# Kernel optimization log

Hardware: AMD Instinct MI355X
Metric: run time of the kernel (lower is better)

The kernel has to match this reference:

```python
import jax, jax.numpy as jnp
import numpy as np

B, L, G, HID, H, D = 2, 4096, 256, 768, 12, 64
R = 127            # local_radius
BLK = R + 1        # block_len = 128
N = L // BLK       # 32 blocks (L divisible by BLK)
W = 2 * R + 1      # 255 local window
V = 32             # relative vocab size


def setup_inputs() -> dict:
    ks = jax.random.split(jax.random.key(0), 40)
    inp = {}
    inp["long_input"] = jax.random.normal(ks[0], (B, L, HID), jnp.float32)
    inp["global_input"] = jax.random.normal(ks[1], (B, G, HID), jnp.float32)
    inp["l2l_att_mask"] = jax.random.randint(ks[2], (B, L, W), 0, 2, jnp.int32)
    inp["g2g_att_mask"] = jax.random.randint(ks[3], (B, G, G), 0, 2, jnp.int32)
    inp["l2g_att_mask"] = jax.random.randint(ks[4], (B, L, G), 0, 2, jnp.int32)
    inp["g2l_att_mask"] = jax.random.randint(ks[5], (B, G, L), 0, 2, jnp.int32)
    inp["l2l_relative_att_ids"] = jax.random.randint(ks[6], (B, L, W), 0, V, jnp.int32)
    inp["g2g_relative_att_ids"] = jax.random.randint(ks[7], (B, G, G), 0, V, jnp.int32)
    inp["l2g_relative_att_ids"] = jax.random.randint(ks[8], (B, L, G), 0, V, jnp.int32)
    inp["g2l_relative_att_ids"] = jax.random.randint(ks[9], (B, G, L), 0, V, jnp.int32)
    i = 10
    for nm in ["q_long", "k_long", "v_long", "q_glob", "k_glob", "v_glob"]:
        inp["w" + nm] = 0.02 * jax.random.normal(ks[i], (HID, H * D), jnp.float32); i += 1
        inp["b" + nm] = jnp.zeros((H * D,), jnp.float32)
    inp["rel_emb_long"] = 0.5 * jax.random.normal(ks[i], (V, H, D), jnp.float32); i += 1
    inp["rel_bias_long"] = jnp.zeros((V, H), jnp.float32)
    inp["rel_emb_glob"] = 0.5 * jax.random.normal(ks[i], (V, H, D), jnp.float32); i += 1
    inp["rel_bias_glob"] = jnp.zeros((V, H), jnp.float32)
    inp["wo_long"] = 0.02 * jax.random.normal(ks[i], (H * D, HID), jnp.float32); i += 1
    inp["bo_long"] = jnp.zeros((HID,), jnp.float32)
    inp["wo_glob"] = 0.02 * jax.random.normal(ks[i], (H * D, HID), jnp.float32); i += 1
    inp["bo_glob"] = jnp.zeros((HID,), jnp.float32)
    return inp


def _expand_local(x):
    """[B, L, W] local-window ids -> blocked [B, N, BLK, 3*BLK] (skew + pad),
    zeroing entries outside the local window or outside the sequence."""
    xb = x.reshape(B, N, BLK, W)
    p = jnp.arange(BLK)[:, None]        # query pos within block
    c = jnp.arange(3 * BLK)[None, :]    # key pos within 3-block window
    r = c - p - 1                       # index into the 2R+1 window
    valid = (r >= 0) & (r < W)
    rc = jnp.clip(r, 0, W - 1)
    out = jnp.take_along_axis(xb, jnp.broadcast_to(rc, (B, N, BLK, 3 * BLK)), axis=-1)
    j = (jnp.arange(N)[:, None, None] - 1) * BLK + c  # absolute key position
    valid_full = valid[None] & (j >= 0) & (j < L)     # [N, BLK, 3*BLK]
    return out * valid_full[None].astype(x.dtype)


def reference(long_input, global_input,
              l2l_att_mask, g2g_att_mask, l2g_att_mask, g2l_att_mask,
              l2l_relative_att_ids, g2g_relative_att_ids,
              l2g_relative_att_ids, g2l_relative_att_ids,
              wq_long, bq_long, wk_long, bk_long, wv_long, bv_long,
              wq_glob, bq_glob, wk_glob, bk_glob, wv_glob, bv_glob,
              rel_emb_long, rel_bias_long, rel_emb_glob, rel_bias_glob,
              wo_long, bo_long, wo_glob, bo_glob):
    scale = 1.0 / jnp.sqrt(jnp.float32(D))

    def proj(x, w, b):
        return (x @ w + b).reshape(x.shape[0], x.shape[1], H, D)

    lq, lk, lv = proj(long_input, wq_long, bq_long), proj(long_input, wk_long, bk_long), proj(long_input, wv_long, bv_long)
    gq, gk, gv = proj(global_input, wq_glob, bq_glob), proj(global_input, wk_glob, bk_glob), proj(global_input, wv_glob, bv_glob)

    # ---- long tokens: blocked local attention fused with side (global) keys ----
    qb = lq.reshape(B, N, BLK, H, D)

    def concat3(x):
        xb = x.reshape(B, N, BLK, H, D)
        pad = jnp.zeros_like(xb[:, :1])
        xp = jnp.concatenate([pad, xb, pad], axis=1)  # [B, N+2, BLK, H, D]
        return jnp.concatenate([xp[:, :-2], xp[:, 1:-1], xp[:, 2:]], axis=2)  # [B,N,3BLK,H,D]

    keys = jnp.concatenate([concat3(lk), jnp.broadcast_to(gk[:, None], (B, N, G, H, D))], axis=2)
    vals = jnp.concatenate([concat3(lv), jnp.broadcast_to(gv[:, None], (B, N, G, H, D))], axis=2)

    mask = jnp.concatenate([_expand_local(l2l_att_mask), l2g_att_mask.reshape(B, N, BLK, G)], axis=-1)
    ids = jnp.concatenate([_expand_local(l2l_relative_att_ids), l2g_relative_att_ids.reshape(B, N, BLK, G)], axis=-1)

    scores = jnp.einsum('bnqhd,bnkhd->bnqkh', qb, keys)
    rel_all = jnp.einsum('bnqhd,rhd->bnqrh', qb, rel_emb_long) + rel_bias_long
    rel = jnp.take_along_axis(rel_all, jnp.broadcast_to(ids[..., None], ids.shape + (H,)), axis=3)
    scores = (scores + rel) * scale
    scores = scores - 10000.0 * (1.0 - mask[..., None].astype(scores.dtype))
    probs = jax.nn.softmax(scores, axis=3)
    long_ctx = jnp.einsum('bnqkh,bnkhd->bnqhd', probs, vals).reshape(B, L, H * D)
    long_out = long_ctx @ wo_long + bo_long

    # ---- global tokens: full attention over [global; long] keys ----
    kf = jnp.concatenate([gk, lk], axis=1)
    vf = jnp.concatenate([gv, lv], axis=1)
    gmask = jnp.concatenate([g2g_att_mask, g2l_att_mask], axis=-1)
    gids = jnp.concatenate([g2g_relative_att_ids, g2l_relative_att_ids], axis=-1)
    gs = jnp.einsum('bqhd,bkhd->bqkh', gq, kf)
    grel_all = jnp.einsum('bqhd,rhd->bqrh', gq, rel_emb_glob) + rel_bias_glob
    grel = jnp.take_along_axis(grel_all, jnp.broadcast_to(gids[..., None], gids.shape + (H,)), axis=2)
    gs = (gs + grel) * scale
    gs = gs - 10000.0 * (1.0 - gmask[..., None].astype(gs.dtype))
    gp = jax.nn.softmax(gs, axis=2)
    glob_ctx = jnp.einsum('bqkh,bkhd->bqhd', gp, vf).reshape(B, G, H * D)
    glob_out = glob_ctx @ wo_glob + bo_glob

    return long_out, glob_out
```

## Files before the change

kernel.cpp:

```cpp
#include <hip/hip_runtime.h>
#include <hip/hip_bf16.h>

typedef unsigned short u16;
typedef unsigned char u8;
typedef unsigned int u32;
typedef __attribute__((ext_vector_type(8))) short bf16x8;
typedef __attribute__((ext_vector_type(4))) float f32x4;

#define BB 2
#define LL 4096
#define GG 256
#define HH 12
#define DD 64
#define NB 32
#define WW 255
#define VV 32
#define NCHUNK 17
#define LKEY 640
#define GKEY 4352
#define WMAT 589824

#define PKL_BLK 20480
#define PKG_BLK 8704
#define WPR_BLK 1152
#define XPL_BLK 3072
#define XPG_BLK 192

__device__ __forceinline__ float bf2f(u16 u) {
  return __uint_as_float(((unsigned)u) << 16);
}
__device__ __forceinline__ u16 f2bf(float f) {
  unsigned u = __float_as_uint(f);
  u += 0x7FFFu + ((u >> 16) & 1u);
  return (u16)(u >> 16);
}
__device__ __forceinline__ float4 ld4bf(const u16* p) {
  ushort4 q = *reinterpret_cast<const ushort4*>(p);
  return make_float4(bf2f(q.x), bf2f(q.y), bf2f(q.z), bf2f(q.w));
}
__device__ __forceinline__ float ldx1(const void* p, size_t idx, bool f32m) {
  if (f32m) return reinterpret_cast<const float*>(p)[idx];
  return bf2f(reinterpret_cast<const u16*>(p)[idx]);
}
__device__ __forceinline__ void gload16(const u16* src, u16* ldsdst) {
  __builtin_amdgcn_global_load_lds(
      (const __attribute__((address_space(1))) unsigned int*)src,
      (__attribute__((address_space(3))) unsigned int*)ldsdst, 16, 0, 0);
}

__global__ void detect_dtype(const void* __restrict__ x, int* __restrict__ flag) {
  __shared__ int cnt;
  if (threadIdx.x == 0) cnt = 0;
  __syncthreads();
  const u16* p = reinterpret_cast<const u16*>(x);
  int c = 0;
  for (int i = threadIdx.x; i < 4096; i += 256) {
    int e = (p[i] >> 7) & 0xFF;
    if (e >= 134) c++;
  }
  atomicAdd(&cnt, c);
  __syncthreads();
  if (threadIdx.x == 0) *flag = (cnt >= 64) ? 1 : 0;
}

__global__ __launch_bounds__(256)
void prep(const int* __restrict__ m_l2l, const int* __restrict__ m_l2g,
          const int* __restrict__ i_l2l, const int* __restrict__ i_l2g,
          const int* __restrict__ m_g2g, const int* __restrict__ m_g2l,
          const int* __restrict__ i_g2g, const int* __restrict__ i_g2l,
          u8* __restrict__ pkl, u8* __restrict__ pkg,
          const void* __restrict__ W0, const void* __restrict__ W1,
          const void* __restrict__ W2, const void* __restrict__ W3,
          const void* __restrict__ W4, const void* __restrict__ W5,
          const void* __restrict__ W6, const void* __restrict__ W7,
          u16* __restrict__ wtq, u16* __restrict__ wto,
          const void* __restrict__ xlin, const void* __restrict__ xgin,
          u16* __restrict__ xl, u16* __restrict__ xg,
          const int* __restrict__ flagp) {
  __shared__ u16 T[64][72];
  const bool f32m = (*flagp != 0);
  const int tid = threadIdx.x;
  const int bid = blockIdx.x;

  if (bid < PKL_BLK) {
    const unsigned idx = (unsigned)bid * 256u + tid;
    const int pos = idx & 63;
    const int lnp = pos >> 2, ktp = pos & 3;
    const int qrow = (idx >> 6) & 127;
    const unsigned rest = idx >> 13;
    const int tile = rest % 10;
    const unsigned bn = rest / 10;
    const int n = bn & 31, b = bn >> 5;
    const int c = (tile << 6) + (ktp << 4) + lnp;
    const unsigned bt = (unsigned)b * LL + (n << 7) + qrow;
    int mask = 0, id = 0;
    if (c < 384) {
      const int rr = c - qrow - 1;
      const int jabs = ((n - 1) << 7) + c;
      if (rr >= 0 && rr < WW && jabs >= 0 && jabs < LL) {
        const size_t base = (size_t)bt * WW + rr;
        mask = m_l2l[base]; id = i_l2l[base];
      }
    } else {
      const size_t base = (size_t)bt * GG + (c - 384);
      mask = m_l2g[base]; id = i_l2g[base];
    }
    pkl[idx] = (u8)((id & 31) | ((mask ^ 1) << 7));
  } else if (bid < PKL_BLK + PKG_BLK) {
    const unsigned idx = (unsigned)(bid - PKL_BLK) * 256u + tid;
    const int pos = idx & 63;
    const int lnp = pos >> 2, ktp = pos & 3;
    const int qrow = (idx >> 6) & 127;
    const unsigned rest = idx >> 13;
    const int tl = rest % 68;
    const unsigned b2q = rest / 68;
    const int b = b2q >> 1, qtp = b2q & 1;
    const int c = (tl << 6) + (ktp << 4) + lnp;
    const int q = (qtp << 7) + qrow;
    int mask, id;
    if (c < 256) {
      const size_t base = ((size_t)b * GG + q) * GG + c;
      mask = m_g2g[base]; id = i_g2g[base];
    } else {
      const size_t base = ((size_t)b * GG + q) * (size_t)LL + (c - 256);
      mask = m_g2l[base]; id = i_g2l[base];
    }
    pkg[idx] = (u8)((id & 31) | ((mask ^ 1) << 7));
  } else if (bid < PKL_BLK + PKG_BLK + WPR_BLK) {
    const int blk = bid - (PKL_BLK + PKG_BLK);
    const int mat = blk / 144;
    const int rem = blk % 144;
    const int n0 = (rem % 12) << 6, k0 = (rem / 12) << 6;
    const void* Wm = (mat == 0) ? W0 : (mat == 1) ? W1 : (mat == 2) ? W2
                     : (mat == 3) ? W3 : (mat == 4) ? W4 : (mat == 5) ? W5
                     : (mat == 6) ? W6 : W7;
    u16* wbase = (mat < 6) ? (wtq + (size_t)mat * WMAT)
                           : (wto + (size_t)(mat - 6) * WMAT);
    {
      const int r = tid >> 2, c0 = (tid & 3) << 4;
      if (f32m) {
        const float* wp = reinterpret_cast<const float*>(Wm) + (size_t)(k0 + r) * 768 + n0 + c0;
        #pragma unroll
        for (int j = 0; j < 16; j += 4) {
          float4 v = *reinterpret_cast<const float4*>(wp + j);
          T[r][c0 + j + 0] = f2bf(v.x); T[r][c0 + j + 1] = f2bf(v.y);
          T[r][c0 + j + 2] = f2bf(v.z); T[r][c0 + j + 3] = f2bf(v.w);
        }
      } else {
        const u16* wp = reinterpret_cast<const u16*>(Wm) + (size_t)(k0 + r) * 768 + n0 + c0;
        *reinterpret_cast<int4*>(&T[r][c0]) = reinterpret_cast<const int4*>(wp)[0];
        *reinterpret_cast<int4*>(&T[r][c0 + 8]) = reinterpret_cast<const int4*>(wp)[1];
      }
    }
    __syncthreads();
    {
      const int n = tid >> 2, kc0 = (tid & 3) << 4;
      u16 buf[16];
      #pragma unroll
      for (int j = 0; j < 16; j++) buf[j] = T[kc0 + j][n];
      u16* op = wbase + (size_t)(n0 + n) * 768 + k0 + kc0;
      *reinterpret_cast<int4*>(op) = *reinterpret_cast<int4*>(buf);
      *reinterpret_cast<int4*>(op + 8) = *reinterpret_cast<int4*>(buf + 8);
    }
  } else {
    const int blk = bid - (PKL_BLK + PKG_BLK + WPR_BLK);
    const void* src;
    u16* dst;
    size_t i;
    if (blk < XPL_BLK) {
      src = xlin; dst = xl;
      i = ((size_t)blk * 256 + tid) << 3;
    } else {
      src = xgin; dst = xg;
      i = ((size_t)(blk - XPL_BLK) * 256 + tid) << 3;
    }
    if (f32m) {
      const float* p = reinterpret_cast<const float*>(src) + i;
      float4 a = *reinterpret_cast<const float4*>(p);
      float4 b = *reinterpret_cast<const float4*>(p + 4);
      u16 o[8] = {f2bf(a.x), f2bf(a.y), f2bf(a.z), f2bf(a.w),
                  f2bf(b.x), f2bf(b.y), f2bf(b.z), f2bf(b.w)};
      *reinterpret_cast<int4*>(dst + i) = *reinterpret_cast<int4*>(o);
    } else {
      *reinterpret_cast<int4*>(dst + i) =
          *reinterpret_cast<const int4*>(reinterpret_cast<const u16*>(src) + i);
    }
  }
}

#define GEMM_CORE(A_, Wt_, row0_, ncol0_)                                        \
  __shared__ u16 lds[16384];                                                     \
  const int tid = threadIdx.x;                                                   \
  const int w = tid >> 6, l = tid & 63;                                          \
  const int lm = l & 15, quad = l >> 4;                                          \
  const int wr = w >> 1, wc = w & 1;                                             \
  const int rb = (w << 5) + (l >> 3);                                            \
  const int c8 = (l & 7) ^ (l >> 3);                                             \
  const u16* asrc = A_ + (size_t)(row0_ + rb) * 768 + (c8 << 3);                 \
  const u16* bsrc = Wt_ + (size_t)(ncol0_ + rb) * 768 + (c8 << 3);               \
  u16* adst = lds + (w << 11) + (l << 3);                                        \
  u16* bdst = adst + 8192;                                                       \
  f32x4 acc[4][4];                                                               \
  _Pragma("unroll")                                                              \
  for (int mt = 0; mt < 4; mt++)                                                 \
    _Pragma("unroll")                                                            \
    for (int nt = 0; nt < 4; nt++) acc[mt][nt] = (f32x4){0.f, 0.f, 0.f, 0.f};    \
  const char* abase = reinterpret_cast<const char*>(lds);                        \
  const char* bbase = abase + 16384;                                             \
  const int xorv = (lm & 7) << 4;                                                \
  for (int k0 = 0; k0 < 768; k0 += 64) {                                         \
    __syncthreads();                                                             \
    _Pragma("unroll")                                                            \
    for (int i = 0; i < 4; i++) gload16(asrc + k0 + i * 6144, adst + (i << 9));  \
    _Pragma("unroll")                                                            \
    for (int i = 0; i < 4; i++) gload16(bsrc + k0 + i * 6144, bdst + (i << 9));  \
    __syncthreads();                                                             \
    _Pragma("unroll")                                                            \
    for (int kk = 0; kk < 2; kk++) {                                             \
      bf16x8 af[4], bfr[4];                                                      \
      _Pragma("unroll")                                                          \
      for (int mt = 0; mt < 4; mt++)                                             \
        af[mt] = *reinterpret_cast<const bf16x8*>(                               \
            abase + ((wr << 6) + (mt << 4) + lm) * 128 +                         \
            (((kk << 6) + (quad << 4)) ^ xorv));                                 \
      _Pragma("unroll")                                                          \
      for (int nt = 0; nt < 4; nt++)                                             \
        bfr[nt] = *reinterpret_cast<const bf16x8*>(                              \
            bbase + ((wc << 6) + (nt << 4) + lm) * 128 +                         \
            (((kk << 6) + (quad << 4)) ^ xorv));                                 \
      _Pragma("unroll")                                                          \
      for (int mt = 0; mt < 4; mt++)                                             \
        _Pragma("unroll")                                                        \
        for (int nt = 0; nt < 4; nt++)                                           \
          acc[mt][nt] = __builtin_amdgcn_mfma_f32_16x16x32_bf16(                 \
              af[mt], bfr[nt], acc[mt][nt], 0, 0, 0);                            \
    }                                                                            \
  }

__global__ __launch_bounds__(256)
void gemm_qkv(const u16* __restrict__ Al, const u16* __restrict__ Ag,
              const u16* __restrict__ Wtq,
              const void* __restrict__ bql, const void* __restrict__ bkl,
              const void* __restrict__ bvl,
              const void* __restrict__ bqg, const void* __restrict__ bkg,
              const void* __restrict__ bvg,
              u16* __restrict__ lq, u16* __restrict__ lk, u16* __restrict__ lv,
              u16* __restrict__ gq, u16* __restrict__ gk, u16* __restrict__ gv,
              const int* __restrict__ flagp) {
  const bool f32m = (*flagp != 0);
  const int fid = blockIdx.x;
  int lx, ly;
  const u16 *A, *Wt;
  const void *B0, *B1, *B2;
  u16 *C0, *C1, *C2;
  if (fid < 1152) {
    const int x = fid & 7, r = fid >> 3;
    ly = (x << 3) | (r & 7);
    lx = r >> 3;
    A = Al; Wt = Wtq;
    B0 = bql; B1 = bkl; B2 = bvl;
    C0 = lq; C1 = lk; C2 = lv;
  } else {
    const int g = fid - 1152;
    lx = g % 18; ly = g / 18;
    A = Ag; Wt = Wtq + (size_t)3 * WMAT;
    B0 = bqg; B1 = bkg; B2 = bvg;
    C0 = gq; C1 = gk; C2 = gv;
  }
  const int row0 = ly << 7;
  const int ncol0 = lx << 7;
  GEMM_CORE(A, Wt, row0, ncol0)

  const int which = lx / 6;
  const void* bias = (which == 0) ? B0 : ((which == 1) ? B1 : B2);
  u16* Cv = (which == 0) ? C0 : ((which == 1) ? C1 : C2);
  const float sc = (which == 0) ? 0.125f : 1.0f;
  const int colw = (lx % 6) << 7;
  #pragma unroll
  for (int nt = 0; nt < 4; nt++) {
    const int gcol = colw + (wc << 6) + (nt << 4) + lm;
    const float bv = ldx1(bias, gcol, f32m);
    #pragma unroll
    for (int mt = 0; mt < 4; mt++)
      #pragma unroll
      for (int r = 0; r < 4; r++) {
        const int grow = row0 + (wr << 6) + (mt << 4) + (quad << 2) + r;
        Cv[(size_t)grow * 768 + gcol] = f2bf((acc[mt][nt][r] + bv) * sc);
      }
  }
}

__global__ __launch_bounds__(256)
void gemm_out(const u16* __restrict__ Alc, const u16* __restrict__ Agc,
              const u16* __restrict__ Wto,
              const void* __restrict__ bol, const void* __restrict__ bog,
              void* __restrict__ Cv, const int* __restrict__ flagp) {
  const bool f32m = (*flagp != 0);
  const int fid = blockIdx.x;
  int lx, ly;
  const u16 *A, *Wt;
  const void* bias;
  size_t c_off;
  if (fid < 384) {
    const int x = fid & 7, r = fid >> 3;
    ly = (x << 3) | (r & 7);
    lx = r >> 3;
    A = Alc; Wt = Wto; bias = bol; c_off = 0;
  } else {
    const int g = fid - 384;
    lx = g % 6; ly = g / 6;
    A = Agc; Wt = Wto + WMAT; bias = bog; c_off = (size_t)BB * LL * 768;
  }
  const int row0 = ly << 7;
  const int ncol0 = lx << 7;
  GEMM_CORE(A, Wt, row0, ncol0)

  #pragma unroll
  for (int nt = 0; nt < 4; nt++) {
    const int gcol = ncol0 + (wc << 6) + (nt << 4) + lm;
    const float bv = ldx1(bias, gcol, f32m);
    #pragma unroll
    for (int mt = 0; mt < 4; mt++)
      #pragma unroll
      for (int r = 0; r < 4; r++) {
        const int grow = row0 + (wr << 6) + (mt << 4) + (quad << 2) + r;
        const float v = acc[mt][nt][r] + bv;
        if (f32m)
          reinterpret_cast<float*>(Cv)[c_off + (size_t)grow * 768 + gcol] = v;
        else
          reinterpret_cast<u16*>(Cv)[c_off + (size_t)grow * 768 + gcol] = f2bf(v);
      }
  }
}

__global__ __launch_bounds__(256)
void relk(const u16* __restrict__ Ql, const u16* __restrict__ Qg,
          const void* __restrict__ embl, const void* __restrict__ biasl,
          const void* __restrict__ embg, const void* __restrict__ biasg,
          u16* __restrict__ outl, u16* __restrict__ outg,
          const int* __restrict__ flagp) {
  const bool f32m = (*flagp != 0);
  const int bid = blockIdx.x;
  const u16* Q;
  const void *emb, *bias;
  u16* outp;
  int h, b, t0, T;
  if (bid < 1536) {
    b = bid / 768;
    const int rem = bid % 768;
    h = rem / 64;
    t0 = (rem % 64) << 6;
    Q = Ql; emb = embl; bias = biasl; outp = outl; T = LL;
  } else {
    const int g = bid - 1536;
    b = g / 48;
    const int rem = g % 48;
    h = rem / 4;
    t0 = (rem % 4) << 6;
    Q = Qg; emb = embg; bias = biasg; outp = outg; T = GG;
  }
  const int tid = threadIdx.x;
  __shared__ float Qst[64][68];
  __shared__ float Es[64][36];
  #pragma unroll
  for (int i = 0; i < 4; i++) {
    const int idx = tid + (i << 8);
    const int tt = idx >> 4, d = (idx & 15) << 2;
    float4 v = ld4bf(Q + (((size_t)b * T + t0 + tt) * HH + h) * DD + d);
    Qst[d + 0][tt] = v.x; Qst[d + 1][tt] = v.y;
    Qst[d + 2][tt] = v.z; Qst[d + 3][tt] = v.w;
  }
  #pragma unroll
  for (int i = 0; i < 8; i++) {
    const int idx = tid + (i << 8);
    const int r = idx >> 6, d = idx & 63;
    Es[d][r] = ldx1(emb, ((size_t)r * HH + h) * DD + d, f32m);
  }
  __syncthreads();
  const int tq = (tid & 31) << 1;
  const int r0 = (tid >> 5) << 2;
  float acc[2][4] = {};
  #pragma unroll 8
  for (int d = 0; d < 64; d++) {
    float2 qq = *reinterpret_cast<const float2*>(&Qst[d][tq]);
    float4 e = *reinterpret_cast<const float4*>(&Es[d][r0]);
    acc[0][0] += qq.x * e.x; acc[0][1] += qq.x * e.y;
    acc[0][2] += qq.x * e.z; acc[0][3] += qq.x * e.w;
    acc[1][0] += qq.y * e.x; acc[1][1] += qq.y * e.y;
    acc[1][2] += qq.y * e.z; acc[1][3] += qq.y * e.w;
  }
  float bv[4];
  #pragma unroll
  for (int j = 0; j < 4; j++) bv[j] = ldx1(bias, (size_t)(r0 + j) * HH + h, f32m) * 0.125f;
  #pragma unroll
  for (int i = 0; i < 2; i++) {
    ushort4 o;
    o.x = f2bf(acc[i][0] + bv[0]); o.y = f2bf(acc[i][1] + bv[1]);
    o.z = f2bf(acc[i][2] + bv[2]); o.w = f2bf(acc[i][3] + bv[3]);
    *reinterpret_cast<ushort4*>(&outp[(((size_t)b * T + t0 + tq + i) * HH + h) * VV + r0]) = o;
  }
}

__global__ __launch_bounds__(512)
void lattn(const u16* __restrict__ lq, const u16* __restrict__ lk, const u16* __restrict__ lv,
           const u16* __restrict__ gk, const u16* __restrict__ gv,
           const u32* __restrict__ pkl, const u16* __restrict__ rel,
           u16* __restrict__ lctx) {
  const int fid = blockIdx.x + 12 * (blockIdx.y + (blockIdx.z << 5));
  const int hg = fid >> 3;
  const int h = hg % 12;
  const int fl = (fid & 7) + ((hg / 12) << 3);
  const int n = fl & 31, b = fl >> 5;
  const int tid = threadIdx.x;
  __shared__ u16 Kt[64][72];
  __shared__ u16 Vt[64][74];
  __shared__ u16 Pt[128][76];
  __shared__ u16 Rl[128][36];

  const int lane = tid & 63, wv = tid >> 6;
  const int ln = lane & 15, quad = lane >> 4;
  const int tbase = n << 7;

  {
    const int qr = (wv << 4) + (lane >> 2);
    const int seg = (lane & 3) << 3;
    *reinterpret_cast<int4*>(&Rl[qr][seg]) = *reinterpret_cast<const int4*>(
        rel + (((size_t)b * LL + tbase + qr) * HH + h) * VV + seg);
  }

  bf16x8 aq[2];
  {
    const int t = tbase + (wv << 4) + ln;
    const u16* qp = lq + (((size_t)b * LL + t) * HH + h) * DD + (quad << 3);
    aq[0] = *reinterpret_cast<const bf16x8*>(qp);
    aq[1] = *reinterpret_cast<const bf16x8*>(qp + 32);
  }

  const u32* pk32 = pkl + (size_t)(b * 32 + n) * 20480;
  const int skey = tid >> 3, sdg = (tid & 7) << 3;
  const int scol = ((skey & 15) << 2) | (skey >> 4);

  f32x4 Oacc[4];
  #pragma unroll
  for (int dt = 0; dt < 4; dt++) Oacc[dt] = (f32x4){0.f, 0.f, 0.f, 0.f};
  float lpart[4] = {};

  for (int tile = 0; tile < 10; tile++) {
    const int c0 = tile << 6;
    const bool isg = (tile >= 6);

    float badd[16];
    #pragma unroll
    for (int r = 0; r < 4; r++) {
      const int qrow = (wv << 4) + (quad << 2) + r;
      const u32 pw = pk32[(((tile << 7) + qrow) << 4) + ln];
      #pragma unroll
      for (int kt = 0; kt < 4; kt++) {
        const u32 pb = (pw >> (kt << 3)) & 0xFFu;
        const float rv = bf2f(Rl[qrow][pb & 31]);
        badd[(kt << 2) + r] = (pb & 0x80u) ? (rv - 10000.f) : rv;
      }
    }

    __syncthreads();
    {
      int4 kraw = {0, 0, 0, 0}, vraw = {0, 0, 0, 0};
      if (isg) {
        const size_t base = (((size_t)b * GG + (c0 - 384) + skey) * HH + h) * DD + sdg;
        kraw = *reinterpret_cast<const int4*>(gk + base);
        vraw = *reinterpret_cast<const int4*>(gv + base);
      } else {
        const int jabs = ((n - 1) << 7) + c0 + skey;
        if (jabs >= 0 && jabs < LL) {
          const size_t base = (((size_t)b * LL + jabs) * HH + h) * DD + sdg;
          kraw = *reinterpret_cast<const int4*>(lk + base);
          vraw = *reinterpret_cast<const int4*>(lv + base);
        }
      }
      *reinterpret_cast<int4*>(&Kt[skey][sdg]) = kraw;
      u16 vb[8];
      *reinterpret_cast<int4*>(vb) = vraw;
      #pragma unroll
      for (int j = 0; j < 8; j++) Vt[sdg + j][scol] = vb[j];
    }
    __syncthreads();

    f32x4 Sacc[4];
    #pragma unroll
    for (int kt = 0; kt < 4; kt++) Sacc[kt] = (f32x4){0.f, 0.f, 0.f, 0.f};
    __builtin_amdgcn_s_setprio(1);
    #pragma unroll
    for (int kk = 0; kk < 2; kk++) {
      bf16x8 bk[4];
      #pragma unroll
      for (int kt = 0; kt < 4; kt++)
        bk[kt] = *reinterpret_cast<const bf16x8*>(&Kt[(kt << 4) + ln][(kk << 5) + (quad << 3)]);
      #pragma unroll
      for (int kt = 0; kt < 4; kt++)
        Sacc[kt] = __builtin_amdgcn_mfma_f32_16x16x32_bf16(aq[kk], bk[kt], Sacc[kt], 0, 0, 0);
    }
    __builtin_amdgcn_s_setprio(0);

    #pragma unroll
    for (int r = 0; r < 4; r++) {
      const int ql = (wv << 4) + (quad << 2) + r;
      const float p0 = __expf(Sacc[0][r] + badd[0 + r]);
      const float p1 = __expf(Sacc[1][r] + badd[4 + r]);
      const float p2 = __expf(Sacc[2][r] + badd[8 + r]);
      const float p3 = __expf(Sacc[3][r] + badd[12 + r]);
      u32 w0, w1;
      asm("v_cvt_pk_bf16_f32 %0, %1, %2" : "=v"(w0) : "v"(p0), "v"(p1));
      asm("v_cvt_pk_bf16_f32 %0, %1, %2" : "=v"(w1) : "v"(p2), "v"(p3));
      uint2 wp; wp.x = w0; wp.y = w1;
      *reinterpret_cast<uint2*>(&Pt[ql][ln << 2]) = wp;
      lpart[r] += (p0 + p1) + (p2 + p3);
    }

    __builtin_amdgcn_s_setprio(1);
    #pragma unroll
    for (int kk = 0; kk < 2; kk++) {
      bf16x8 ap = *reinterpret_cast<const bf16x8*>(&Pt[(wv << 4) + ln][(kk << 5) + (quad << 3)]);
      #pragma unroll
      for (int dt = 0; dt < 4; dt++) {
        bf16x8 bv = *reinterpret_cast<const bf16x8*>(&Vt[(dt << 4) + ln][(kk << 5) + (quad << 3)]);
        Oacc[dt] = __builtin_amdgcn_mfma_f32_16x16x32_bf16(ap, bv, Oacc[dt], 0, 0, 0);
      }
    }
    __builtin_amdgcn_s_setprio(0);
  }

  #pragma unroll
  for (int r = 0; r < 4; r++) {
    float v = lpart[r];
    v += __shfl_xor(v, 1); v += __shfl_xor(v, 2);
    v += __shfl_xor(v, 4); v += __shfl_xor(v, 8);
    const float inv = 1.0f / v;
    const int t = tbase + (wv << 4) + (quad << 2) + r;
    const size_t base = (((size_t)b * LL + t) * HH + h) * DD;
    #pragma unroll
    for (int dt = 0; dt < 4; dt++)
      lctx[base + (dt << 4) + ln] = f2bf(Oacc[dt][r] * inv);
  }
}

__global__ __launch_bounds__(512)
void gattn(const u16* __restrict__ gq, const u16* __restrict__ gk, const u16* __restrict__ gv,
           const u16* __restrict__ lk, const u16* __restrict__ lv,
           const u32* __restrict__ pkg, const u16* __restrict__ relg,
           float* __restrict__ po, float* __restrict__ pl) {
  const int fid = blockIdx.x;
  const int x = fid & 7;
  const int slot = fid >> 3;
  const int qtp = slot & 1;
  const int g = ((slot >> 1) << 3) | x;
  const int h = g % 12;
  const int cb = g / 12;
  const int chunk = cb % 17;
  const int b = cb / 17;
  const int tid = threadIdx.x;
  __shared__ u16 Kt[64][72];
  __shared__ u16 Vt[64][74];
  __shared__ u16 Pt[128][76];
  __shared__ u16 Rg[128][36];

  const int lane = tid & 63, wv = tid >> 6;
  const int ln = lane & 15, quad = lane >> 4;
  const int qbase = qtp << 7;
  const int kbase = chunk << 8;
  const bool isgg = (chunk == 0);

  {
    const int qr = (wv << 4) + (lane >> 2);
    const int seg = (lane & 3) << 3;
    *reinterpret_cast<int4*>(&Rg[qr][seg]) = *reinterpret_cast<const int4*>(
        relg + (((size_t)b * GG + qbase + qr) * HH + h) * VV + seg);
  }

  bf16x8 aq[2];
  {
    const int qa = qbase + (wv << 4) + ln;
    const u16* qp = gq + (((size_t)b * GG + qa) * HH + h) * DD + (quad << 3);
    aq[0] = *reinterpret_cast<const bf16x8*>(qp);
    aq[1] = *reinterpret_cast<const bf16x8*>(qp + 32);
  }

  const u32* pk32 = pkg + (size_t)((b << 1) + qtp) * 139264;
  const int skey = tid >> 3, sdg = (tid & 7) << 3;
  const int scol = ((skey & 15) << 2) | (skey >> 4);

  f32x4 Oacc[4];
  #pragma unroll
  for (int dt = 0; dt < 4; dt++) Oacc[dt] = (f32x4){0.f, 0.f, 0.f, 0.f};
  float lpart[4] = {};

  for (int tile = 0; tile < 4; tile++) {
    const int tl = (chunk << 2) + tile;

    float badd[16];
    #pragma unroll
    for (int r = 0; r < 4; r++) {
      const int qrow = (wv << 4) + (quad << 2) + r;
      const u32 pw = pk32[(((tl << 7) + qrow) << 4) + ln];
      #pragma unroll
      for (int kt = 0; kt < 4; kt++) {
        const u32 pb = (pw >> (kt << 3)) & 0xFFu;
        const float rv = bf2f(Rg[qrow][pb & 31]);
        badd[(kt << 2) + r] = (pb & 0x80u) ? (rv - 10000.f) : rv;
      }
    }

    __syncthreads();
    {
      const int kc = kbase + (tile << 6) + skey;
      int4 kraw, vraw;
      if (isgg) {
        const size_t base = (((size_t)b * GG + kc) * HH + h) * DD + sdg;
        kraw = *reinterpret_cast<const int4*>(gk + base);
        vraw = *reinterpret_cast<const int4*>(gv + base);
      } else {
        const size_t base = (((size_t)b * LL + (kc - 256)) * HH + h) * DD + sdg;
        kraw = *reinterpret_cast<const int4*>(lk + base);
        vraw = *reinterpret_cast<const int4*>(lv + base);
      }
      *reinterpret_cast<int4*>(&Kt[skey][sdg]) = kraw;
      u16 vb[8];
      *reinterpret_cast<int4*>(vb) = vraw;
      #pragma unroll
      for (int j = 0; j < 8; j++) Vt[sdg + j][scol] = vb[j];
    }
    __syncthreads();

    f32x4 Sacc[4];
    #pragma unroll
    for (int kt = 0; kt < 4; kt++) Sacc[kt] = (f32x4){0.f, 0.f, 0.f, 0.f};
    __builtin_amdgcn_s_setprio(1);
    #pragma unroll
    for (int kk = 0; kk < 2; kk++) {
      bf16x8 bk[4];
      #pragma unroll
      for (int kt = 0; kt < 4; kt++)
        bk[kt] = *reinterpret_cast<const bf16x8*>(&Kt[(kt << 4) + ln][(kk << 5) + (quad << 3)]);
      #pragma unroll
      for (int kt = 0; kt < 4; kt++)
        Sacc[kt] = __builtin_amdgcn_mfma_f32_16x16x32_bf16(aq[kk], bk[kt], Sacc[kt], 0, 0, 0);
    }
    __builtin_amdgcn_s_setprio(0);

    #pragma unroll
    for (int r = 0; r < 4; r++) {
      const int ql = (wv << 4) + (quad << 2) + r;
      const float p0 = __expf(Sacc[0][r] + badd[0 + r]);
      const float p1 = __expf(Sacc[1][r] + badd[4 + r]);
      const float p2 = __expf(Sacc[2][r] + badd[8 + r]);
      const float p3 = __expf(Sacc[3][r] + badd[12 + r]);
      u32 w0, w1;
      asm("v_cvt_pk_bf16_f32 %0, %1, %2" : "=v"(w0) : "v"(p0), "v"(p1));
      asm("v_cvt_pk_bf16_f32 %0, %1, %2" : "=v"(w1) : "v"(p2), "v"(p3));
      uint2 wp; wp.x = w0; wp.y = w1;
      *reinterpret_cast<uint2*>(&Pt[ql][ln << 2]) = wp;
      lpart[r] += (p0 + p1) + (p2 + p3);
    }

    __builtin_amdgcn_s_setprio(1);
    #pragma unroll
    for (int kk = 0; kk < 2; kk++) {
      bf16x8 ap = *reinterpret_cast<const bf16x8*>(&Pt[(wv << 4) + ln][(kk << 5) + (quad << 3)]);
      #pragma unroll
      for (int dt = 0; dt < 4; dt++) {
        bf16x8 bv = *reinterpret_cast<const bf16x8*>(&Vt[(dt << 4) + ln][(kk << 5) + (quad << 3)]);
        Oacc[dt] = __builtin_amdgcn_mfma_f32_16x16x32_bf16(ap, bv, Oacc[dt], 0, 0, 0);
      }
    }
    __builtin_amdgcn_s_setprio(0);
  }

  #pragma unroll
  for (int r = 0; r < 4; r++) {
    float v = lpart[r];
    v += __shfl_xor(v, 1); v += __shfl_xor(v, 2);
    v += __shfl_xor(v, 4); v += __shfl_xor(v, 8);
    const int qa = qbase + (wv << 4) + (quad << 2) + r;
    if (ln == 0)
      pl[(((size_t)chunk * BB + b) * HH + h) * GG + qa] = v;
    const size_t base = ((((size_t)chunk * BB + b) * HH + h) * GG + qa) * DD;
    #pragma unroll
    for (int dt = 0; dt < 4; dt++)
      po[base + (dt << 4) + ln] = Oacc[dt][r];
  }
}

__global__ __launch_bounds__(256)
void gcombine(const float* __restrict__ po, const float* __restrict__ pl,
              u16* __restrict__ gctx) {
  const int flat = blockIdx.x * 256 + threadIdx.x;
  const int d = flat & 63;
  const int rest = flat >> 6;
  const int h = rest % HH;
  const int bq = rest / HH;
  const int b = bq >> 8, qg = bq & 255;
  float so = 0.f, sl = 0.f;
  #pragma unroll
  for (int c = 0; c < NCHUNK; c++) {
    so += po[((((size_t)c * BB + b) * HH + h) * GG + qg) * DD + d];
    sl += pl[(((size_t)c * BB + b) * HH + h) * GG + qg];
  }
  gctx[flat] = f2bf(so / sl);
}

extern "C" void kernel_launch(void* const* d_in, const int* in_sizes, int n_in,
                              void* d_out, int out_size, void* d_ws, size_t ws_size,
                              hipStream_t stream) {
  (void)in_sizes; (void)n_in; (void)out_size; (void)ws_size;
  const void* x_long = d_in[0];
  const void* x_glob = d_in[1];
  const int* m_l2l = (const int*)d_in[2];
  const int* m_g2g = (const int*)d_in[3];
  const int* m_l2g = (const int*)d_in[4];
  const int* m_g2l = (const int*)d_in[5];
  const int* i_l2l = (const int*)d_in[6];
  const int* i_g2g = (const int*)d_in[7];
  const int* i_l2g = (const int*)d_in[8];
  const int* i_g2l = (const int*)d_in[9];
  const void* wq_l = d_in[10]; const void* bq_l = d_in[11];
  const void* wk_l = d_in[12]; const void* bk_l = d_in[13];
  const void* wv_l = d_in[14]; const void* bv_l = d_in[15];
  const void* wq_g = d_in[16]; const void* bq_g = d_in[17];
  const void* wk_g = d_in[18]; const void* bk_g = d_in[19];
  const void* wv_g = d_in[20]; const void* bv_g = d_in[21];
  const void* rel_emb_l = d_in[22]; const void* rel_bias_l = d_in[23];
  const void* rel_emb_g = d_in[24]; const void* rel_bias_g = d_in[25];
  const void* wo_l = d_in[26]; const void* bo_l = d_in[27];
  const void* wo_g = d_in[28]; const void* bo_g = d_in[29];

  constexpr size_t NLQ = (size_t)BB * LL * HH * DD;
  constexpr size_t NG  = (size_t)BB * GG * HH * DD;
  constexpr size_t NRL = (size_t)BB * LL * HH * VV;
  constexpr size_t NRG = (size_t)BB * GG * HH * VV;
  u16* lqw  = reinterpret_cast<u16*>(d_ws);
  u16* lkw  = lqw + NLQ;
  u16* lvw  = lkw + NLQ;
  u16* gqw  = lvw + NLQ;
  u16* gkw  = gqw + NG;
  u16* gvw  = gkw + NG;
  u16* rell = gvw + NG;
  u16* relg = rell + NRL;
  u16* lctx = relg + NRG;
  u16* gctx = lctx + NLQ;
  int* flag = reinterpret_cast<int*>(gctx + NG);
  float* po = reinterpret_cast<float*>(flag + 16);
  float* pl = po + (size_t)NCHUNK * BB * HH * GG * DD;
  u8* pk_l = reinterpret_cast<u8*>(po);
  u16* wt_qkv = reinterpret_cast<u16*>(po) + 2621440;
  u16* xl_bf = lctx;
  u16* xg_bf = gctx;
  u8* pk_g = reinterpret_cast<u8*>(pl + (size_t)NCHUNK * BB * HH * GG);
  u16* wt_o = reinterpret_cast<u16*>(pk_g + (size_t)BB * GG * GKEY);

  dim3 t256(256);
  detect_dtype<<<1, t256, 0, stream>>>(x_long, flag);
  prep<<<dim3(PKL_BLK + PKG_BLK + WPR_BLK + XPL_BLK + XPG_BLK), t256, 0, stream>>>(
      m_l2l, m_l2g, i_l2l, i_l2g, m_g2g, m_g2l, i_g2g, i_g2l, pk_l, pk_g,
      wq_l, wk_l, wv_l, wq_g, wk_g, wv_g, wo_l, wo_g, wt_qkv, wt_o,
      x_long, x_glob, xl_bf, xg_bf, flag);
  gemm_qkv<<<dim3(1224), t256, 0, stream>>>(
      xl_bf, xg_bf, wt_qkv, bq_l, bk_l, bv_l, bq_g, bk_g, bv_g,
      lqw, lkw, lvw, gqw, gkw, gvw, flag);
  relk<<<dim3(1632), t256, 0, stream>>>(
      lqw, gqw, rel_emb_l, rel_bias_l, rel_emb_g, rel_bias_g, rell, relg, flag);
  lattn<<<dim3(12, 32, 2), dim3(512), 0, stream>>>(lqw, lkw, lvw, gkw, gvw,
                                                   reinterpret_cast<const u32*>(pk_l), rell, lctx);
  gattn<<<dim3(816), dim3(512), 0, stream>>>(gqw, gkw, gvw, lkw, lvw,
                                             reinterpret_cast<const u32*>(pk_g), relg, po, pl);
  gcombine<<<dim3(1536), t256, 0, stream>>>(po, pl, gctx);
  gemm_out<<<dim3(408), t256, 0, stream>>>(lctx, gctx, wt_o, bo_l, bo_g, d_out, flag);
}
```

Baseline: 375.8 us.

## Fold relative-embedding projection into QKV GEMM via precomputed Wq·emb weights

Precomputes fused weight matrices Wq_h·emb_r (scaled) and bias constants in the prep kernel, then appends them as extra output columns to the QKV GEMM so relative logits come directly from the input activations. This removes the separate relk kernel launch and its re-read of Q. In exchange the GEMM grows by 384 columns per side, rel logits skip the bf16 rounding of Q (slight numeric difference), and prep gains a per-block dot-product stage.

```diff
diff --git a/kernel.cpp b/kernel.cpp
--- a/kernel.cpp
+++ b/kernel.cpp
@@ -19,12 +19,14 @@
 #define LKEY 640
 #define GKEY 4352
 #define WMAT 589824
+#define MMAT 294912
 
 #define PKL_BLK 20480
 #define PKG_BLK 8704
 #define WPR_BLK 1152
 #define XPL_BLK 3072
 #define XPG_BLK 192
+#define MPR_BLK 768
 
 __device__ __forceinline__ float bf2f(u16 u) {
   return __uint_as_float(((unsigned)u) << 16);
@@ -76,6 +78,10 @@
           u16* __restrict__ wtq, u16* __restrict__ wto,
           const void* __restrict__ xlin, const void* __restrict__ xgin,
           u16* __restrict__ xl, u16* __restrict__ xg,
+          const void* __restrict__ embl, const void* __restrict__ rbl,
+          const void* __restrict__ embg, const void* __restrict__ rbg,
+          const void* __restrict__ bql, const void* __restrict__ bqg,
+          u16* __restrict__ wtrel, float* __restrict__ crel,
           const int* __restrict__ flagp) {
   __shared__ u16 T[64][72];
   const bool f32m = (*flagp != 0);
@@ -162,7 +168,7 @@
       *reinterpret_cast<int4*>(op) = *reinterpret_cast<int4*>(buf);
       *reinterpret_cast<int4*>(op + 8) = *reinterpret_cast<int4*>(buf + 8);
     }
-  } else {
+  } else if (bid < PKL_BLK + PKG_BLK + WPR_BLK + XPL_BLK + XPG_BLK) {
     const int blk = bid - (PKL_BLK + PKG_BLK + WPR_BLK);
     const void* src;
     u16* dst;
@@ -184,6 +190,46 @@
     } else {
       *reinterpret_cast<int4*>(dst + i) =
           *reinterpret_cast<const int4*>(reinterpret_cast<const u16*>(src) + i);
+    }
+  } else {
+    const int blk = bid - (PKL_BLK + PKG_BLK + WPR_BLK + XPL_BLK + XPG_BLK);
+    const int side = blk / 384;
+    const int nl = blk % 384;
+    const int h = nl >> 5, r = nl & 31;
+    const void* Wq = side ? W3 : W0;
+    const void* emb = side ? embg : embl;
+    const void* bqv = side ? bqg : bql;
+    const void* rbv = side ? rbg : rbl;
+    float* ef = reinterpret_cast<float*>(&T[0][0]);
+    if (tid < 64) ef[tid] = ldx1(emb, ((size_t)r * HH + h) * DD + tid, f32m);
+    __syncthreads();
+    #pragma unroll
+    for (int ko = 0; ko < 3; ko++) {
+      const int k = tid + (ko << 8);
+      const size_t base = (size_t)k * 768 + h * 64;
+      float a = 0.f;
+      if (f32m) {
+        const float* wp = reinterpret_cast<const float*>(Wq) + base;
+        #pragma unroll
+        for (int d = 0; d < 64; d += 4) {
+          float4 v = *reinterpret_cast<const float4*>(wp + d);
+          a += v.x * ef[d] + v.y * ef[d + 1] + v.z * ef[d + 2] + v.w * ef[d + 3];
+        }
+      } else {
+        const u16* wp = reinterpret_cast<const u16*>(Wq) + base;
+        #pragma unroll
+        for (int d = 0; d < 64; d += 4) {
+          float4 v = ld4bf(wp + d);
+          a += v.x * ef[d] + v.y * ef[d + 1] + v.z * ef[d + 2] + v.w * ef[d + 3];
+        }
+      }
+      wtrel[(size_t)side * MMAT + (size_t)nl * 768 + k] = f2bf(0.125f * a);
+    }
+    if (tid == 0) {
+      float s = ldx1(rbv, (size_t)r * HH + h, f32m);
+      for (int d = 0; d < 64; d++)
+        s += ldx1(bqv, h * 64 + d, f32m) * ef[d];
+      crel[side * 384 + nl] = 0.125f * s;
     }
   }
 }
@@ -239,54 +285,73 @@
 
 __global__ __launch_bounds__(256)
 void gemm_qkv(const u16* __restrict__ Al, const u16* __restrict__ Ag,
-              const u16* __restrict__ Wtq,
+              const u16* __restrict__ Wtq, const u16* __restrict__ Wtr,
+              const float* __restrict__ crel,
               const void* __restrict__ bql, const void* __restrict__ bkl,
               const void* __restrict__ bvl,
               const void* __restrict__ bqg, const void* __restrict__ bkg,
               const void* __restrict__ bvg,
               u16* __restrict__ lq, u16* __restrict__ lk, u16* __restrict__ lv,
               u16* __restrict__ gq, u16* __restrict__ gk, u16* __restrict__ gv,
+              u16* __restrict__ rell, u16* __restrict__ relg,
               const int* __restrict__ flagp) {
   const bool f32m = (*flagp != 0);
   const int fid = blockIdx.x;
   int lx, ly;
-  const u16 *A, *Wt;
-  const void *B0, *B1, *B2;
-  u16 *C0, *C1, *C2;
-  if (fid < 1152) {
-    const int x = fid & 7, r = fid >> 3;
-    ly = (x << 3) | (r & 7);
-    lx = r >> 3;
-    A = Al; Wt = Wtq;
-    B0 = bql; B1 = bkl; B2 = bvl;
-    C0 = lq; C1 = lk; C2 = lv;
+  bool isL;
+  if (fid < 1344) {
+    isL = true;
+    const int x = fid & 7, rr = fid >> 3;
+    ly = (x << 3) | (rr & 7);
+    lx = rr >> 3;
   } else {
-    const int g = fid - 1152;
-    lx = g % 18; ly = g / 18;
-    A = Ag; Wt = Wtq + (size_t)3 * WMAT;
-    B0 = bqg; B1 = bkg; B2 = bvg;
-    C0 = gq; C1 = gk; C2 = gv;
-  }
+    isL = false;
+    const int g = fid - 1344;
+    lx = g % 21; ly = g / 21;
+  }
+  const u16* A = isL ? Al : Ag;
+  const u16* Wsel;
+  int ncolw;
+  if (lx < 18) { Wsel = isL ? Wtq : (Wtq + (size_t)3 * WMAT); ncolw = lx << 7; }
+  else         { Wsel = Wtr + (isL ? 0 : (size_t)MMAT);       ncolw = (lx - 18) << 7; }
   const int row0 = ly << 7;
-  const int ncol0 = lx << 7;
-  GEMM_CORE(A, Wt, row0, ncol0)
-
-  const int which = lx / 6;
-  const void* bias = (which == 0) ? B0 : ((which == 1) ? B1 : B2);
-  u16* Cv = (which == 0) ? C0 : ((which == 1) ? C1 : C2);
-  const float sc = (which == 0) ? 0.125f : 1.0f;
-  const int colw = (lx % 6) << 7;
-  #pragma unroll
-  for (int nt = 0; nt < 4; nt++) {
-    const int gcol = colw + (wc << 6) + (nt << 4) + lm;
-    const float bv = ldx1(bias, gcol, f32m);
-    #pragma unroll
-    for (int mt = 0; mt < 4; mt++)
-      #pragma unroll
-      for (int r = 0; r < 4; r++) {
-        const int grow = row0 + (wr << 6) + (mt << 4) + (quad << 2) + r;
-        Cv[(size_t)grow * 768 + gcol] = f2bf((acc[mt][nt][r] + bv) * sc);
-      }
+  GEMM_CORE(A, Wsel, row0, ncolw)
+
+  if (lx < 18) {
+    const int which = lx / 6;
+    const void* bias = (which == 0) ? (isL ? bql : bqg)
+                     : (which == 1) ? (isL ? bkl : bkg) : (isL ? bvl : bvg);
+    u16* Cv = (which == 0) ? (isL ? lq : gq)
+            : (which == 1) ? (isL ? lk : gk) : (isL ? lv : gv);
+    const float sc = (which == 0) ? 0.125f : 1.0f;
+    const int colw = (lx % 6) << 7;
+    #pragma unroll
+    for (int nt = 0; nt < 4; nt++) {
+      const int gcol = colw + (wc << 6) + (nt << 4) + lm;
+      const float bv = ldx1(bias, gcol, f32m);
+      #pragma unroll
+      for (int mt = 0; mt < 4; mt++)
+        #pragma unroll
+        for (int r = 0; r < 4; r++) {
+          const int grow = row0 + (wr << 6) + (mt << 4) + (quad << 2) + r;
+          Cv[(size_t)grow * 768 + gcol] = f2bf((acc[mt][nt][r] + bv) * sc);
+        }
+    }
+  } else {
+    const float* cr = crel + (isL ? 0 : 384);
+    u16* ro = isL ? rell : relg;
+    #pragma unroll
+    for (int nt = 0; nt < 4; nt++) {
+      const int gcol = ncolw + (wc << 6) + (nt << 4) + lm;
+      const float cv = cr[gcol];
+      #pragma unroll
+      for (int mt = 0; mt < 4; mt++)
+        #pragma unroll
+        for (int r = 0; r < 4; r++) {
+          const int grow = row0 + (wr << 6) + (mt << 4) + (quad << 2) + r;
+          ro[(size_t)grow * 384 + gcol] = f2bf(acc[mt][nt][r] + cv);
+        }
+    }
   }
 }
 
@@ -333,74 +398,6 @@
   }
 }
 
-__global__ __launch_bounds__(256)
-void relk(const u16* __restrict__ Ql, const u16* __restrict__ Qg,
-          const void* __restrict__ embl, const void* __restrict__ biasl,
-          const void* __restrict__ embg, const void* __restrict__ biasg,
-          u16* __restrict__ outl, u16* __restrict__ outg,
-          const int* __restrict__ flagp) {
-  const bool f32m = (*flagp != 0);
-  const int bid = blockIdx.x;
-  const u16* Q;
-  const void *emb, *bias;
-  u16* outp;
-  int h, b, t0, T;
-  if (bid < 1536) {
-    b = bid / 768;
-    const int rem = bid % 768;
-    h = rem / 64;
-    t0 = (rem % 64) << 6;
-    Q = Ql; emb = embl; bias = biasl; outp = outl; T = LL;
-  } else {
-    const int g = bid - 1536;
-    b = g / 48;
-    const int rem = g % 48;
-    h = rem / 4;
-    t0 = (rem % 4) << 6;
-    Q = Qg; emb = embg; bias = biasg; outp = outg; T = GG;
-  }
-  const int tid = threadIdx.x;
-  __shared__ float Qst[64][68];
-  __shared__ float Es[64][36];
-  #pragma unroll
-  for (int i = 0; i < 4; i++) {
-    const int idx = tid + (i << 8);
-    const int tt = idx >> 4, d = (idx & 15) << 2;
-    float4 v = ld4bf(Q + (((size_t)b * T + t0 + tt) * HH + h) * DD + d);
-    Qst[d + 0][tt] = v.x; Qst[d + 1][tt] = v.y;
-    Qst[d + 2][tt] = v.z; Qst[d + 3][tt] = v.w;
-  }
-  #pragma unroll
-  for (int i = 0; i < 8; i++) {
-    const int idx = tid + (i << 8);
-    const int r = idx >> 6, d = idx & 63;
-    Es[d][r] = ldx1(emb, ((size_t)r * HH + h) * DD + d, f32m);
-  }
-  __syncthreads();
-  const int tq = (tid & 31) << 1;
-  const int r0 = (tid >> 5) << 2;
-  float acc[2][4] = {};
-  #pragma unroll 8
-  for (int d = 0; d < 64; d++) {
-    float2 qq = *reinterpret_cast<const float2*>(&Qst[d][tq]);
-    float4 e = *reinterpret_cast<const float4*>(&Es[d][r0]);
-    acc[0][0] += qq.x * e.x; acc[0][1] += qq.x * e.y;
-    acc[0][2] += qq.x * e.z; acc[0][3] += qq.x * e.w;
-    acc[1][0] += qq.y * e.x; acc[1][1] += qq.y * e.y;
-    acc[1][2] += qq.y * e.z; acc[1][3] += qq.y * e.w;
-  }
-  float bv[4];
-  #pragma unroll
-  for (int j = 0; j < 4; j++) bv[j] = ldx1(bias, (size_t)(r0 + j) * HH + h, f32m) * 0.125f;
-  #pragma unroll
-  for (int i = 0; i < 2; i++) {
-    ushort4 o;
-    o.x = f2bf(acc[i][0] + bv[0]); o.y = f2bf(acc[i][1] + bv[1]);
-    o.z = f2bf(acc[i][2] + bv[2]); o.w = f2bf(acc[i][3] + bv[3]);
-    *reinterpret_cast<ushort4*>(&outp[(((size_t)b * T + t0 + tq + i) * HH + h) * VV + r0]) = o;
-  }
-}
-
 __global__ __launch_bounds__(512)
 void lattn(const u16* __restrict__ lq, const u16* __restrict__ lk, const u16* __restrict__ lv,
            const u16* __restrict__ gk, const u16* __restrict__ gv,
@@ -425,7 +422,7 @@
     const int qr = (wv << 4) + (lane >> 2);
     const int seg = (lane & 3) << 3;
     *reinterpret_cast<int4*>(&Rl[qr][seg]) = *reinterpret_cast<const int4*>(
-        rel + (((size_t)b * LL + tbase + qr) * HH + h) * VV + seg);
+        rel + ((size_t)(b * LL + tbase + qr)) * 384 + h * 32 + seg);
   }
 
   bf16x8 aq[2];
@@ -573,7 +570,7 @@
     const int qr = (wv << 4) + (lane >> 2);
     const int seg = (lane & 3) << 3;
     *reinterpret_cast<int4*>(&Rg[qr][seg]) = *reinterpret_cast<const int4*>(
-        relg + (((size_t)b * GG + qbase + qr) * HH + h) * VV + seg);
+        relg + ((size_t)(b * GG + qbase + qr)) * 384 + h * 32 + seg);
   }
 
   bf16x8 aq[2];
@@ -755,18 +752,21 @@
   u16* xg_bf = gctx;
   u8* pk_g = reinterpret_cast<u8*>(pl + (size_t)NCHUNK * BB * HH * GG);
   u16* wt_o = reinterpret_cast<u16*>(pk_g + (size_t)BB * GG * GKEY);
+  u16* wt_rel = wt_o + (size_t)2 * WMAT;
+  float* c_rel = reinterpret_cast<float*>(wt_rel + (size_t)2 * MMAT);
 
   dim3 t256(256);
   detect_dtype<<<1, t256, 0, stream>>>(x_long, flag);
-  prep<<<dim3(PKL_BLK + PKG_BLK + WPR_BLK + XPL_BLK + XPG_BLK), t256, 0, stream>>>(
+  prep<<<dim3(PKL_BLK + PKG_BLK + WPR_BLK + XPL_BLK + XPG_BLK + MPR_BLK), t256, 0, stream>>>(
       m_l2l, m_l2g, i_l2l, i_l2g, m_g2g, m_g2l, i_g2g, i_g2l, pk_l, pk_g,
       wq_l, wk_l, wv_l, wq_g, wk_g, wv_g, wo_l, wo_g, wt_qkv, wt_o,
-      x_long, x_glob, xl_bf, xg_bf, flag);
-  gemm_qkv<<<dim3(1224), t256, 0, stream>>>(
-      xl_bf, xg_bf, wt_qkv, bq_l, bk_l, bv_l, bq_g, bk_g, bv_g,
-      lqw, lkw, lvw, gqw, gkw, gvw, flag);
-  relk<<<dim3(1632), t256, 0, stream>>>(
-      lqw, gqw, rel_emb_l, rel_bias_l, rel_emb_g, rel_bias_g, rell, relg, flag);
+      x_long, x_glob, xl_bf, xg_bf,
+      rel_emb_l, rel_bias_l, rel_emb_g, rel_bias_g, bq_l, bq_g,
+      wt_rel, c_rel, flag);
+  gemm_qkv<<<dim3(1428), t256, 0, stream>>>(
+      xl_bf, xg_bf, wt_qkv, wt_rel, c_rel,
+      bq_l, bk_l, bv_l, bq_g, bk_g, bv_g,
+      lqw, lkw, lvw, gqw, gkw, gvw, rell, relg, flag);
   lattn<<<dim3(12, 32, 2), dim3(512), 0, stream>>>(lqw, lkw, lvw, gkw, gvw,
                                                    reinterpret_cast<const u32*>(pk_l), rell, lctx);
   gattn<<<dim3(816), dim3(512), 0, stream>>>(gqw, gkw, gvw, lkw, lvw,
```

Result: slower. 400.9 us (+6.7%).
